# Optimization experiments

Hardware: AMD Instinct MI355X
Metric: run time of the kernel (lower is better)

## Reference

```python
import jax, jax.numpy as jnp
import numpy as np
import math

D_MODEL = 1024
EXPAND = 2
D_INNER = EXPAND * D_MODEL        # 2048
HEADDIM = 64
NHEADS = D_INNER // HEADDIM       # 32
D_STATE = 128
D_CONV = 4
CHUNK = 128
SEQLEN = 4096
BATCH = 1                         # bidirectional merge in forward hard-codes batch=1
CONV_DIM = D_INNER + 2 * (2 * D_STATE)            # 2560
D_IN_PROJ = 2 * D_INNER + 2 * (2 * D_STATE) + 2 * NHEADS  # 4672
EPS = 1e-5


def silu(x):
    return x * jax.nn.sigmoid(x)


def segsum_exp(a):
    """exp(segsum(a)): out[..., i, j] = exp(sum_{k=j+1..i} a[..., k]) for i>=j else 0."""
    T = a.shape[-1]
    m1 = jnp.tril(jnp.ones((T, T), bool), -1)
    s = jnp.cumsum(jnp.where(m1, a[..., :, None], 0.0), axis=-2)
    m0 = jnp.tril(jnp.ones((T, T), bool))
    return jnp.where(m0, jnp.exp(jnp.where(m0, s, 0.0)), 0.0)


def ssd(x, A, B, C, chunk):
    """x:(b,L,h,p) A:(b,L,h) B,C:(b,L,n) (head dim of size 1 squeezed). L % chunk == 0."""
    b, L, h, p = x.shape
    c = L // chunk
    x = x.reshape(b, c, chunk, h, p)
    A = A.reshape(b, c, chunk, h).transpose(0, 3, 1, 2)   # (b,h,c,l)
    B = B.reshape(b, c, chunk, -1)
    C = C.reshape(b, c, chunk, -1)
    A_cs = jnp.cumsum(A, axis=-1)                          # (b,h,c,l)
    Lmat = segsum_exp(A)                                   # (b,h,c,l,l)
    # intra-chunk (diagonal block) outputs
    Y_diag = jnp.einsum('bcln,bcsn,bhcls,bcshp->bclhp', C, B, Lmat, x)
    # per-chunk states
    decay_states = jnp.exp(A_cs[..., -1:] - A_cs)          # (b,h,c,l)
    states = jnp.einsum('bcln,bhcl,bclhp->bchpn', B, decay_states, x)
    states = jnp.concatenate([jnp.zeros_like(states[:, :1]), states], axis=1)
    # inter-chunk recurrence via segsum over chunk boundaries
    decay_chunk = segsum_exp(jnp.pad(A_cs[..., -1], ((0, 0), (0, 0), (1, 0))))  # (b,h,c+1,c+1)
    new_states = jnp.einsum('bhzc,bchpn->bzhpn', decay_chunk, states)
    states, final_state = new_states[:, :-1], new_states[:, -1]
    Y_off = jnp.einsum('bcln,bchpn,bhcl->bclhp', C, states, jnp.exp(A_cs))
    Y = (Y_diag + Y_off).reshape(b, L, h, p)
    return Y, final_state


def setup_inputs() -> dict:
    key = jax.random.key(0)
    ks = jax.random.split(key, 8)
    s = 0.02
    u = jax.random.normal(ks[0], (BATCH, SEQLEN, D_MODEL), jnp.float32)
    in_proj_w = jax.random.normal(ks[1], (D_IN_PROJ, D_MODEL), jnp.float32) * s
    conv_w = jax.random.normal(ks[2], (CONV_DIM, 1, D_CONV), jnp.float32) * (1.0 / math.sqrt(D_CONV))
    conv_b = jnp.zeros((CONV_DIM,), jnp.float32)
    dt = jnp.exp(jax.random.uniform(ks[3], (NHEADS,)) * (math.log(0.1) - math.log(0.001)) + math.log(0.001))
    dt = jnp.clip(dt, 1e-4)
    dt_bias = dt + jnp.log(-jnp.expm1(-dt))
    A_log = jnp.log(jax.random.uniform(ks[4], (NHEADS,), minval=1.0, maxval=16.0))
    D = jnp.ones((NHEADS,), jnp.float32)
    fc_D_w = jax.random.normal(ks[5], (NHEADS, D_INNER), jnp.float32) * s
    norm_w = jnp.ones((D_INNER,), jnp.float32)
    out_proj_w = jax.random.normal(ks[6], (D_MODEL, D_INNER), jnp.float32) * s
    return dict(u=u, in_proj_w=in_proj_w, conv_w=conv_w, conv_b=conv_b, dt_bias=dt_bias,
                A_log=A_log, D=D, fc_D_w=fc_D_w, norm_w=norm_w, out_proj_w=out_proj_w)


def reference(u, in_proj_w, conv_w, conv_b, dt_bias, A_log, D, fc_D_w, norm_w, out_proj_w):
    b, l, _ = u.shape
    zxbcdt = u @ in_proj_w.T                               # (b,l,D_IN_PROJ)
    z = zxbcdt[..., :D_INNER]
    xBC = zxbcdt[..., D_INNER:D_INNER + CONV_DIM]
    dt = zxbcdt[..., D_INNER + CONV_DIM:]                  # (b,l,2*nheads)
    # fwd heads + time-reversed bwd heads stacked on batch dim
    dt = jnp.concatenate([dt[..., :NHEADS], jnp.flip(dt[..., NHEADS:], axis=1)], axis=0)
    dt = jax.nn.softplus(dt + dt_bias)                     # (2b,l,nheads)
    # depthwise causal conv1d + silu
    xc = jnp.transpose(xBC, (0, 2, 1))                     # (b,CONV_DIM,l)
    xc = jax.lax.conv_general_dilated(xc, conv_w, (1,), [(D_CONV - 1, 0)],
                                      feature_group_count=CONV_DIM,
                                      dimension_numbers=('NCH', 'OIH', 'NCH'))
    xc = xc + conv_b[None, :, None]
    xBC = silu(jnp.transpose(xc, (0, 2, 1)))               # (b,l,CONV_DIM)
    x = xBC[..., :D_INNER]
    BC = xBC[..., D_INNER:]
    x_og = x
    x2 = jnp.concatenate([x, jnp.flip(x, 1)], axis=0)      # (2b,l,d_inner)
    BC = jnp.concatenate([BC[..., :2 * D_STATE], jnp.flip(BC[..., 2 * D_STATE:], 1)], axis=0)
    B = BC[..., :D_STATE]
    C = BC[..., D_STATE:]
    xh = x2.reshape(2 * b, l, NHEADS, HEADDIM)
    A = -jnp.exp(A_log)
    Y, final_state = ssd(xh * dt[..., None], A * dt, B, C, CHUNK)
    y = Y + xh * D[:, None]
    y = y.reshape(2 * b, l, D_INNER)
    # torch.roll(shift=1, dim=1) then zero first step == shift right with zero pad
    y = jnp.concatenate([jnp.zeros_like(y[:, :1]), y[:, :-1]], axis=1)
    y_fw, y_bw = y[:b], jnp.flip(y[b:], 1)
    fd = x_og @ fc_D_w.T + D                               # F.linear(x_og, fc_D.weight, bias=D)
    y = y_fw + y_bw + x_og * jnp.repeat(fd, HEADDIM, axis=-1)
    # gated RMSNorm
    yg = y * silu(z)
    yn = yg * jax.lax.rsqrt(jnp.mean(yg * yg, axis=-1, keepdims=True) + EPS) * norm_w
    return yn @ out_proj_w.T
```

## Files before the change

kernel.cpp:

```cpp
#include <hip/hip_runtime.h>
#include <hip/hip_bf16.h>
#include <math.h>

#define L_SEQ   4096
#define DMODEL  1024
#define DINNER  2048
#define NHEADS  32
#define HEADDIM 64
#define DSTATE  128
#define NCHUNK  32
#define CHUNKL  128
#define CONVDIM 2560
#define DPROJ   4672
#define NPAD2   4864

typedef __hip_bfloat16 bf16;
__device__ __forceinline__ float b2f(bf16 x) { return __bfloat162float(x); }
__device__ __forceinline__ bf16 f2b(float x) { return __float2bfloat16(x); }
__device__ __forceinline__ float sh2f(short s) {
  return __uint_as_float(((unsigned int)(unsigned short)s) << 16);
}
__device__ __forceinline__ short f2bs(float x) {
  bf16 t = __float2bfloat16(x);
  return *reinterpret_cast<short*>(&t);
}

typedef __attribute__((ext_vector_type(8))) short bf16x8v;
typedef __attribute__((ext_vector_type(4))) float f32x4v;

__device__ __forceinline__ float dot8(bf16x8v x, float4 w0, float4 w1) {
  return sh2f(x[0]) * w0.x + sh2f(x[1]) * w0.y + sh2f(x[2]) * w0.z + sh2f(x[3]) * w0.w +
         sh2f(x[4]) * w1.x + sh2f(x[5]) * w1.y + sh2f(x[6]) * w1.z + sh2f(x[7]) * w1.w;
}


__global__ __launch_bounds__(256) void cast2_kernel(
    const float* __restrict__ u, const float* __restrict__ w1,
    bf16* __restrict__ u_bf, bf16* __restrict__ w1_bf) {
  const int NU = (L_SEQ * DMODEL) / 256;
  int bid = blockIdx.x;
  if (bid < NU) {
    int i = bid * 256 + threadIdx.x;
    u_bf[i] = f2b(u[i]);
  } else {
    int i = (bid - NU) * 256 + threadIdx.x;
    w1_bf[i] = (i < DPROJ * DMODEL) ? f2b(w1[i]) : f2b(0.f);
  }
}

__global__ __launch_bounds__(256) void cast_kernel(
    const float* __restrict__ src, bf16* __restrict__ dst, int n_src, int n_tot) {
  int i = blockIdx.x * 256 + threadIdx.x;
  if (i < n_tot) dst[i] = (i < n_src) ? f2b(src[i]) : f2b(0.f);
}

#define G1_K  1024
#define G1_GN 19
#define G1_NT (G1_K / 64)

__global__ __launch_bounds__(512, 2) void gemm1_8ph(
    const bf16* __restrict__ A, const bf16* __restrict__ B, bf16* __restrict__ C) {
  __shared__ bf16 Al[2][2][8192];
  __shared__ bf16 Bl[2][2][8192];
  const int tid = threadIdx.x;
  const int lane = tid & 63;
  const int w = tid >> 6;
  const int wm = w >> 2;
  const int wn = w & 3;
  const int bm = (blockIdx.x / G1_GN) * 256;
  const int bn = (blockIdx.x % G1_GN) * 256;
  const int scol = ((lane & 3) ^ (((lane >> 5) & 1) << 1)) * 8;
  const int cin = ((lane >> 4) * 8) ^ (((lane >> 3) & 1) << 4);
  const int r16 = lane & 15;
  const bf16* Ag = A + (size_t)bm * G1_K;
  const bf16* Bg = B + (size_t)bn * G1_K;

  auto stage = [&](int mat, int tt, int hf) {
    const bf16* g = (mat ? Bg : Ag)
        + (size_t)(hf * 128 + (w >> 1) * 16 + (lane >> 2)) * G1_K
        + tt * 64 + (w & 1) * 32 + scol;
    bf16* d0 = mat ? &Bl[tt & 1][hf][0] : &Al[tt & 1][hf][0];
    __builtin_amdgcn_global_load_lds(
        (const __attribute__((address_space(1))) void*)g,
        (__attribute__((address_space(3))) void*)(d0 + w * 512), 16, 0, 0);
    __builtin_amdgcn_global_load_lds(
        (const __attribute__((address_space(1))) void*)(g + (size_t)64 * G1_K),
        (__attribute__((address_space(3))) void*)(d0 + (8 + w) * 512), 16, 0, 0);
  };

  f32x4v acc[8][4];
#pragma unroll
  for (int i = 0; i < 8; i++)
#pragma unroll
    for (int j = 0; j < 4; j++) acc[i][j] = (f32x4v){0.f, 0.f, 0.f, 0.f};

  stage(0, 0, 0); stage(0, 0, 1); stage(1, 0, 0); stage(1, 0, 1);
  stage(0, 1, 0); stage(0, 1, 1); stage(1, 1, 0);
  asm volatile("s_waitcnt vmcnt(6)" ::: "memory");
  __builtin_amdgcn_s_barrier();
  __builtin_amdgcn_sched_barrier(0);

#pragma unroll 2
  for (int t = 0; t < G1_NT; ++t) {
    const int slot = t & 1;
    const bf16* Ah = &Al[slot][wm][0];
    const bf16* Bh = &Bl[slot][wn >> 1][0];
    const int brb = (wn & 1) * 4;
    bf16x8v a[4][2], b[4][2];
#pragma unroll
    for (int i = 0; i < 4; i++) {
      a[i][0] = *(const bf16x8v*)&Ah[(i * 2 + 0) * 512 + r16 * 32 + cin];
      a[i][1] = *(const bf16x8v*)&Ah[(i * 2 + 1) * 512 + r16 * 32 + cin];
    }
#pragma unroll
    for (int j = 0; j < 2; j++) {
      b[j][0] = *(const bf16x8v*)&Bh[((brb + j) * 2 + 0) * 512 + r16 * 32 + cin];
      b[j][1] = *(const bf16x8v*)&Bh[((brb + j) * 2 + 1) * 512 + r16 * 32 + cin];
    }
    if (t + 1 < G1_NT) stage(1, t + 1, 1);
    __builtin_amdgcn_s_barrier();
    asm volatile("s_waitcnt lgkmcnt(0)" ::: "memory");
    __builtin_amdgcn_s_setprio(1);
#pragma unroll
    for (int i = 0; i < 4; i++)
#pragma unroll
      for (int j = 0; j < 2; j++) {
        acc[i][j] = __builtin_amdgcn_mfma_f32_16x16x32_bf16(a[i][0], b[j][0], acc[i][j], 0, 0, 0);
        acc[i][j] = __builtin_amdgcn_mfma_f32_16x16x32_bf16(a[i][1], b[j][1], acc[i][j], 0, 0, 0);
      }
    __builtin_amdgcn_s_setprio(0);
    __builtin_amdgcn_s_barrier();
#pragma unroll
    for (int j = 2; j < 4; j++) {
      b[j][0] = *(const bf16x8v*)&Bh[((brb + j) * 2 + 0) * 512 + r16 * 32 + cin];
      b[j][1] = *(const bf16x8v*)&Bh[((brb + j) * 2 + 1) * 512 + r16 * 32 + cin];
    }
    __builtin_amdgcn_s_barrier();
    asm volatile("s_waitcnt lgkmcnt(0)" ::: "memory");
    __builtin_amdgcn_s_setprio(1);
#pragma unroll
    for (int i = 0; i < 4; i++)
#pragma unroll
      for (int j = 2; j < 4; j++) {
        acc[i][j] = __builtin_amdgcn_mfma_f32_16x16x32_bf16(a[i][0], b[j][0], acc[i][j], 0, 0, 0);
        acc[i][j] = __builtin_amdgcn_mfma_f32_16x16x32_bf16(a[i][1], b[j][1], acc[i][j], 0, 0, 0);
      }
    __builtin_amdgcn_s_setprio(0);
    __builtin_amdgcn_s_barrier();
#pragma unroll
    for (int i = 0; i < 4; i++) {
      a[i][0] = *(const bf16x8v*)&Ah[((4 + i) * 2 + 0) * 512 + r16 * 32 + cin];
      a[i][1] = *(const bf16x8v*)&Ah[((4 + i) * 2 + 1) * 512 + r16 * 32 + cin];
    }
    if (t + 2 < G1_NT) stage(1, t + 2, 0);
    __builtin_amdgcn_s_barrier();
    asm volatile("s_waitcnt lgkmcnt(0)" ::: "memory");
    __builtin_amdgcn_s_setprio(1);
#pragma unroll
    for (int i = 0; i < 4; i++)
#pragma unroll
      for (int j = 2; j < 4; j++) {
        acc[4 + i][j] = __builtin_amdgcn_mfma_f32_16x16x32_bf16(a[i][0], b[j][0], acc[4 + i][j], 0, 0, 0);
        acc[4 + i][j] = __builtin_amdgcn_mfma_f32_16x16x32_bf16(a[i][1], b[j][1], acc[4 + i][j], 0, 0, 0);
      }
    __builtin_amdgcn_s_setprio(0);
    __builtin_amdgcn_s_barrier();
    if (t + 2 < G1_NT) { stage(0, t + 2, 0); stage(0, t + 2, 1); }
    __builtin_amdgcn_s_barrier();
    __builtin_amdgcn_s_setprio(1);
#pragma unroll
    for (int i = 0; i < 4; i++)
#pragma unroll
      for (int j = 0; j < 2; j++) {
        acc[4 + i][j] = __builtin_amdgcn_mfma_f32_16x16x32_bf16(a[i][0], b[j][0], acc[4 + i][j], 0, 0, 0);
        acc[4 + i][j] = __builtin_amdgcn_mfma_f32_16x16x32_bf16(a[i][1], b[j][1], acc[4 + i][j], 0, 0, 0);
      }
    __builtin_amdgcn_s_setprio(0);
    if (t < G1_NT - 2)       asm volatile("s_waitcnt vmcnt(6)" ::: "memory");
    else if (t == G1_NT - 2) asm volatile("s_waitcnt vmcnt(0)" ::: "memory");
    __builtin_amdgcn_s_barrier();
    __builtin_amdgcn_sched_barrier(0);
  }

  const int quad = lane >> 4;
  const int cn = lane & 15;
#pragma unroll
  for (int i = 0; i < 8; i++)
#pragma unroll
    for (int j = 0; j < 4; j++) {
      int col = bn + wn * 64 + j * 16 + cn;
      if (col < DPROJ) {
#pragma unroll
        for (int r = 0; r < 4; r++) {
          int row = bm + wm * 128 + i * 16 + quad * 4 + r;
          C[(size_t)row * DPROJ + col] = f2b(acc[i][j][r]);
        }
      }
    }
}

template <typename TC>
__global__ __launch_bounds__(256) void gemm_mfma(
    const bf16* __restrict__ A, int lda,
    const bf16* __restrict__ B, int ldb,
    TC* __restrict__ C, int ldc,
    int N, int K, int gridM, int gridN, int swz) {
  __shared__ short As[128][32];
  __shared__ short Bs[128][32];
  int tid = threadIdx.x;
  int lane = tid & 63;
  int w = tid >> 6;
  int wr = w >> 1, wc = w & 1;
  int bid = blockIdx.x;
  int bm, bn;
  if (swz) {
    int mst = gridM >> 3;
    int xk = bid & 7, q = bid >> 3;
    bm = (xk + 8 * (q % mst)) * 128;
    bn = (q / mst) * 128;
  } else {
    bm = (bid / gridN) * 128;
    bn = (bid % gridN) * 128;
  }
  f32x4v acc[4][4];
#pragma unroll
  for (int i = 0; i < 4; i++)
#pragma unroll
    for (int j = 0; j < 4; j++) acc[i][j] = (f32x4v){0.f, 0.f, 0.f, 0.f};

  const bf16* Ab = A + (size_t)(bm + w * 32 + (lane >> 2)) * lda + (lane & 3) * 8;
  const bf16* Bb = B + (size_t)(bn + w * 32 + (lane >> 2)) * ldb + (lane & 3) * 8;

  for (int k0 = 0; k0 < K; k0 += 32) {
    __builtin_amdgcn_global_load_lds(
        (const __attribute__((address_space(1))) void*)(Ab + k0),
        (__attribute__((address_space(3))) void*)&As[w * 32][0], 16, 0, 0);
    __builtin_amdgcn_global_load_lds(
        (const __attribute__((address_space(1))) void*)(Ab + (size_t)16 * lda + k0),
        (__attribute__((address_space(3))) void*)&As[w * 32 + 16][0], 16, 0, 0);
    __builtin_amdgcn_global_load_lds(
        (const __attribute__((address_space(1))) void*)(Bb + k0),
        (__attribute__((address_space(3))) void*)&Bs[w * 32][0], 16, 0, 0);
    __builtin_amdgcn_global_load_lds(
        (const __attribute__((address_space(1))) void*)(Bb + (size_t)16 * ldb + k0),
        (__attribute__((address_space(3))) void*)&Bs[w * 32 + 16][0], 16, 0, 0);
    __syncthreads();
    bf16x8v af[4], bv[4];
#pragma unroll
    for (int i = 0; i < 4; i++)
      af[i] = *(const bf16x8v*)&As[wr * 64 + i * 16 + (lane & 15)][(lane >> 4) * 8];
#pragma unroll
    for (int j = 0; j < 4; j++)
      bv[j] = *(const bf16x8v*)&Bs[wc * 64 + j * 16 + (lane & 15)][(lane >> 4) * 8];
#pragma unroll
    for (int i = 0; i < 4; i++)
#pragma unroll
      for (int j = 0; j < 4; j++)
        acc[i][j] = __builtin_amdgcn_mfma_f32_16x16x32_bf16(af[i], bv[j], acc[i][j], 0, 0, 0);
    __syncthreads();
  }
  int quad = lane >> 4;
  int cn = lane & 15;
#pragma unroll
  for (int i = 0; i < 4; i++) {
#pragma unroll
    for (int j = 0; j < 4; j++) {
      int col = bn + wc * 64 + j * 16 + cn;
      if (col < N) {
#pragma unroll
        for (int r = 0; r < 4; r++) {
          int row = bm + wr * 64 + i * 16 + quad * 4 + r;
          float v = acc[i][j][r];
          if constexpr (sizeof(TC) == 2) C[(size_t)row * ldc + col] = f2b(v);
          else                           C[(size_t)row * ldc + col] = v;
        }
      }
    }
  }
}

__global__ __launch_bounds__(256) void fc_kernel(
    const bf16* __restrict__ xbc, const float* __restrict__ Wf,
    const float* __restrict__ Dp, float* __restrict__ fd) {
  int lane = threadIdx.x & 63;
  int w = threadIdx.x >> 6;
  int t0 = (blockIdx.x * 4 + w) * 4;
  int h = lane & 31;
  int g = lane >> 5;
  const float* wr = Wf + (size_t)h * DINNER + g * 1024;
  const bf16* xr = xbc + (size_t)t0 * CONVDIM + g * 1024;
  float a0 = 0.f, a1 = 0.f, a2 = 0.f, a3 = 0.f;
  for (int k = 0; k < 1024; k += 8) {
    float4 w0 = *(const float4*)(wr + k);
    float4 w1 = *(const float4*)(wr + k + 4);
    bf16x8v x0 = *(const bf16x8v*)(xr + k);
    bf16x8v x1 = *(const bf16x8v*)(xr + CONVDIM + k);
    bf16x8v x2 = *(const bf16x8v*)(xr + 2 * CONVDIM + k);
    bf16x8v x3 = *(const bf16x8v*)(xr + 3 * CONVDIM + k);
    a0 += dot8(x0, w0, w1);
    a1 += dot8(x1, w0, w1);
    a2 += dot8(x2, w0, w1);
    a3 += dot8(x3, w0, w1);
  }
  a0 += __shfl_down(a0, 32);
  a1 += __shfl_down(a1, 32);
  a2 += __shfl_down(a2, 32);
  a3 += __shfl_down(a3, 32);
  if (lane < 32) {
    float d = Dp[h];
    fd[(t0 + 0) * NHEADS + h] = a0 + d;
    fd[(t0 + 1) * NHEADS + h] = a1 + d;
    fd[(t0 + 2) * NHEADS + h] = a2 + d;
    fd[(t0 + 3) * NHEADS + h] = a3 + d;
  }
}

#define CONV_BLOCKS ((L_SEQ / 4) * CONVDIM / 256)
__global__ __launch_bounds__(256) void conv_dt_kernel(
    const bf16* __restrict__ zx, const float* __restrict__ conv_w,
    const float* __restrict__ conv_b, bf16* __restrict__ xbc,
    const float* __restrict__ dt_bias, float* __restrict__ dt2) {
  int bid = blockIdx.x;
  if (bid < CONV_BLOCKS) {
    int idx = bid * 256 + threadIdx.x;
    int ch = idx % CONVDIM;
    int t0 = (idx / CONVDIM) * 4;
    const bf16* col = zx + DINNER + ch;
    float w0 = conv_w[ch * 4 + 0], w1 = conv_w[ch * 4 + 1];
    float w2 = conv_w[ch * 4 + 2], w3 = conv_w[ch * 4 + 3];
    float bsv = conv_b[ch];
    float x[7];
#pragma unroll
    for (int i = 0; i < 7; i++) {
      int t = t0 - 3 + i;
      x[i] = (t >= 0) ? b2f(col[(size_t)t * DPROJ]) : 0.f;
    }
#pragma unroll
    for (int j = 0; j < 4; j++) {
      float acc = bsv + w0 * x[j] + w1 * x[j + 1] + w2 * x[j + 2] + w3 * x[j + 3];
      xbc[(size_t)(t0 + j) * CONVDIM + ch] = f2b(acc / (1.f + __expf(-acc)));
    }
  } else {
    int idx = (bid - CONV_BLOCKS) * 256 + threadIdx.x;
    int h = idx % NHEADS;
    int t = (idx / NHEADS) % L_SEQ;
    int b = idx / (NHEADS * L_SEQ);
    float v;
    if (b == 0) v = b2f(zx[(size_t)t * DPROJ + 4608 + h]);
    else        v = b2f(zx[(size_t)(L_SEQ - 1 - t) * DPROJ + 4608 + NHEADS + h]);
    v += dt_bias[h];
    dt2[idx] = (v > 20.f) ? v : log1pf(expf(v));
  }
}

__global__ __launch_bounds__(256) void gmat_kernel(
    const bf16* __restrict__ xbc, bf16* __restrict__ G) {
  __shared__ bf16 Cs[32][136];
  __shared__ bf16 Bs[128][136];
  int blk = blockIdx.x;
  int quarter = blk & 3;
  int bc = blk >> 2;
  int b = bc / NCHUNK, c = bc % NCHUNK;
  int l0 = quarter * 32;
  int tid = threadIdx.x;
  int lane = tid & 63;
  int w = tid >> 6;
  int bofs = b ? 2304 : 2048;
  int cofs = b ? 2432 : 2176;
  for (int o = tid; o < CHUNKL * DSTATE / 8; o += 256) {
    int s = o >> 4;
    int n8 = (o & 15) * 8;
    int t = b ? (L_SEQ - 1 - (c * CHUNKL + s)) : (c * CHUNKL + s);
    *(bf16x8v*)&Bs[s][n8] = *(const bf16x8v*)&xbc[(size_t)t * CONVDIM + bofs + n8];
  }
  for (int o = tid; o < 32 * DSTATE / 8; o += 256) {
    int l = o >> 4;
    int n8 = (o & 15) * 8;
    int t = b ? (L_SEQ - 1 - (c * CHUNKL + l0 + l)) : (c * CHUNKL + l0 + l);
    *(bf16x8v*)&Cs[l][n8] = *(const bf16x8v*)&xbc[(size_t)t * CONVDIM + cofs + n8];
  }
  __syncthreads();
  if (w > quarter) return;
  f32x4v acc[2][2];
#pragma unroll
  for (int i = 0; i < 2; i++)
#pragma unroll
    for (int j = 0; j < 2; j++) acc[i][j] = (f32x4v){0.f, 0.f, 0.f, 0.f};
#pragma unroll
  for (int k0 = 0; k0 < 128; k0 += 32) {
    bf16x8v a0 = *(const bf16x8v*)&Cs[(lane & 15)][(lane >> 4) * 8 + k0];
    bf16x8v a1 = *(const bf16x8v*)&Cs[16 + (lane & 15)][(lane >> 4) * 8 + k0];
#pragma unroll
    for (int j = 0; j < 2; j++) {
      bf16x8v bv = *(const bf16x8v*)&Bs[(2 * w + j) * 16 + (lane & 15)][(lane >> 4) * 8 + k0];
      acc[0][j] = __builtin_amdgcn_mfma_f32_16x16x32_bf16(a0, bv, acc[0][j], 0, 0, 0);
      acc[1][j] = __builtin_amdgcn_mfma_f32_16x16x32_bf16(a1, bv, acc[1][j], 0, 0, 0);
    }
  }
  int quad = lane >> 4, cn = lane & 15;
  bf16* Gb = G + (size_t)bc * CHUNKL * CHUNKL;
#pragma unroll
  for (int i = 0; i < 2; i++)
#pragma unroll
    for (int j = 0; j < 2; j++)
#pragma unroll
      for (int r = 0; r < 4; r++) {
        int l = l0 + i * 16 + quad * 4 + r;
        int s = (2 * w + j) * 16 + cn;
        Gb[l * CHUNKL + s] = f2b(acc[i][j][r]);
      }
}

__global__ __launch_bounds__(256) void chunk_kernel(
    const bf16* __restrict__ xbc, const float* __restrict__ dt2,
    const float* __restrict__ A_log,
    bf16* __restrict__ states, float* __restrict__ csum) {
  int gid = blockIdx.x;
  int h = gid % NHEADS;
  int bc = gid / NHEADS;
  int c = bc % NCHUNK, b = bc / NCHUNK;
  int tid = threadIdx.x;
  int lane = tid & 63;
  int w = tid >> 6;
  __shared__ bf16 BdT[128][136];
  __shared__ bf16 xdtT[64][136];
  __shared__ float acs[CHUNKL];
  __shared__ float dtl[CHUNKL];
  __shared__ float decays[CHUNKL];
  if (tid < CHUNKL)
    dtl[tid] = dt2[((size_t)b * L_SEQ + c * CHUNKL + tid) * NHEADS + h];
  __syncthreads();
  if (tid == 0) {
    float Ah = -__expf(A_log[h]);
    float s = 0.f;
    for (int l = 0; l < CHUNKL; l++) { s += Ah * dtl[l]; acs[l] = s; }
    csum[gid] = __expf(s);
  }
  __syncthreads();
  if (tid < CHUNKL) decays[tid] = __expf(acs[CHUNKL - 1] - acs[tid]);
  for (int o = tid; o < CHUNKL * HEADDIM / 8; o += 256) {
    int s = o & 127;
    int p8 = (o >> 7) * 8;
    int t = b ? (L_SEQ - 1 - (c * CHUNKL + s)) : (c * CHUNKL + s);
    bf16x8v xv = *(const bf16x8v*)&xbc[(size_t)t * CONVDIM + h * HEADDIM + p8];
    float d = dtl[s];
#pragma unroll
    for (int j = 0; j < 8; j++) xdtT[p8 + j][s] = f2b(sh2f(xv[j]) * d);
  }
  __syncthreads();
  for (int o = tid; o < CHUNKL * CHUNKL / 8; o += 256) {
    int l = o & 127;
    int n8 = (o >> 7) * 8;
    int t = b ? (L_SEQ - 1 - (c * CHUNKL + l)) : (c * CHUNKL + l);
    bf16x8v bv = *(const bf16x8v*)&xbc[(size_t)t * CONVDIM + (b ? 2304 : 2048) + n8];
    float d = decays[l];
#pragma unroll
    for (int j = 0; j < 8; j++) BdT[n8 + j][l] = f2b(sh2f(bv[j]) * d);
  }
  __syncthreads();
  f32x4v accS[8];
#pragma unroll
  for (int j = 0; j < 8; j++) accS[j] = (f32x4v){0.f, 0.f, 0.f, 0.f};
#pragma unroll
  for (int k0 = 0; k0 < 128; k0 += 32) {
    bf16x8v av = *(const bf16x8v*)&xdtT[w * 16 + (lane & 15)][(lane >> 4) * 8 + k0];
#pragma unroll
    for (int j = 0; j < 8; j++) {
      bf16x8v bv = *(const bf16x8v*)&BdT[j * 16 + (lane & 15)][(lane >> 4) * 8 + k0];
      accS[j] = __builtin_amdgcn_mfma_f32_16x16x32_bf16(av, bv, accS[j], 0, 0, 0);
    }
  }
  int quad = lane >> 4, cn = lane & 15;
  bf16* st = states + (size_t)gid * (HEADDIM * DSTATE);
#pragma unroll
  for (int j = 0; j < 8; j++)
#pragma unroll
    for (int r = 0; r < 4; r++) {
      int p = w * 16 + quad * 4 + r;
      int n = j * 16 + cn;
      st[p * DSTATE + n] = f2b(accS[j][r]);
    }
}

__global__ __launch_bounds__(256) void scan_kernel(
    bf16* __restrict__ states, const float* __restrict__ csum) {
  int idx = blockIdx.x * 256 + threadIdx.x;
  int n = idx % DSTATE;
  int p = (idx / DSTATE) % HEADDIM;
  int h = (idx / (DSTATE * HEADDIM)) % NHEADS;
  int b = idx / (DSTATE * HEADDIM * NHEADS);
  size_t base = ((size_t)(b * NCHUNK) * NHEADS + h) * (HEADDIM * DSTATE) + p * DSTATE + n;
  const size_t cstride = (size_t)NHEADS * HEADDIM * DSTATE;
  float tmp[NCHUNK], cv[NCHUNK];
#pragma unroll
  for (int c = 0; c < NCHUNK; c++) tmp[c] = b2f(states[base + c * cstride]);
#pragma unroll
  for (int c = 0; c < NCHUNK; c++) cv[c] = csum[(b * NCHUNK + c) * NHEADS + h];
  float S = 0.f;
#pragma unroll
  for (int c = 0; c < NCHUNK; c++) {
    states[base + c * cstride] = f2b(S);
    S = cv[c] * S + tmp[c];
  }
}

__global__ __launch_bounds__(256) void yoff_kernel(
    const bf16* __restrict__ xbc, const float* __restrict__ dt2,
    const float* __restrict__ A_log, const bf16* __restrict__ G,
    const bf16* __restrict__ states, const float* __restrict__ Dp,
    bf16* __restrict__ Y) {
  int gid = blockIdx.x;
  int h = gid % NHEADS;
  int bc = gid / NHEADS;
  int c = bc % NCHUNK, b = bc / NCHUNK;
  int tid = threadIdx.x;
  int lane = tid & 63;
  int w = tid >> 6;
  __shared__ bf16 WB[128][136];
  __shared__ bf16 SX[64][136];
  __shared__ float acs[CHUNKL];
  __shared__ float dtl[CHUNKL];
  __shared__ float eAl[CHUNKL];
  if (tid < CHUNKL)
    dtl[tid] = dt2[((size_t)b * L_SEQ + c * CHUNKL + tid) * NHEADS + h];
  __syncthreads();
  if (tid == 0) {
    float Ah = -__expf(A_log[h]);
    float s = 0.f;
    for (int l = 0; l < CHUNKL; l++) { s += Ah * dtl[l]; acs[l] = s; }
  }
  __syncthreads();
  if (tid < CHUNKL) eAl[tid] = __expf(acs[tid]);
  for (int o = tid; o < CHUNKL * HEADDIM / 8; o += 256) {
    int s = o & 127;
    int p8 = (o >> 7) * 8;
    int t = b ? (L_SEQ - 1 - (c * CHUNKL + s)) : (c * CHUNKL + s);
    bf16x8v xv = *(const bf16x8v*)&xbc[(size_t)t * CONVDIM + h * HEADDIM + p8];
    float d = dtl[s];
#pragma unroll
    for (int j = 0; j < 8; j++) SX[p8 + j][s] = f2b(sh2f(xv[j]) * d);
  }
  {
    const bf16* Gb = G + (size_t)bc * CHUNKL * CHUNKL;
    for (int o = tid; o < CHUNKL * CHUNKL / 8; o += 256) {
      int l = o >> 4;
      int s8 = (o & 15) * 8;
      bf16x8v g = *(const bf16x8v*)&Gb[l * CHUNKL + s8];
      float al = acs[l];
      bf16x8v wv;
#pragma unroll
      for (int j = 0; j < 8; j++) {
        int s = s8 + j;
        float e = (s <= l) ? sh2f(g[j]) * __expf(al - acs[s]) : 0.f;
        wv[j] = f2bs(e);
      }
      *(bf16x8v*)&WB[l][s8] = wv;
    }
  }
  __syncthreads();
  f32x4v accY[2][4];
#pragma unroll
  for (int i = 0; i < 2; i++)
#pragma unroll
    for (int j = 0; j < 4; j++) accY[i][j] = (f32x4v){0.f, 0.f, 0.f, 0.f};
#pragma unroll
  for (int k0 = 0; k0 < 128; k0 += 32) {
    bf16x8v a0 = *(const bf16x8v*)&WB[w * 32 + (lane & 15)][(lane >> 4) * 8 + k0];
    bf16x8v a1 = *(const bf16x8v*)&WB[w * 32 + 16 + (lane & 15)][(lane >> 4) * 8 + k0];
#pragma unroll
    for (int j = 0; j < 4; j++) {
      bf16x8v bv = *(const bf16x8v*)&SX[j * 16 + (lane & 15)][(lane >> 4) * 8 + k0];
      accY[0][j] = __builtin_amdgcn_mfma_f32_16x16x32_bf16(a0, bv, accY[0][j], 0, 0, 0);
      accY[1][j] = __builtin_amdgcn_mfma_f32_16x16x32_bf16(a1, bv, accY[1][j], 0, 0, 0);
    }
  }
  __syncthreads();
  {
    int cofs = b ? 2432 : 2176;
    for (int o = tid; o < CHUNKL * DSTATE / 8; o += 256) {
      int l = o >> 4;
      int n8 = (o & 15) * 8;
      int t = b ? (L_SEQ - 1 - (c * CHUNKL + l)) : (c * CHUNKL + l);
      bf16x8v cv = *(const bf16x8v*)&xbc[(size_t)t * CONVDIM + cofs + n8];
      float e = eAl[l];
      bf16x8v ov;
#pragma unroll
      for (int j = 0; j < 8; j++) ov[j] = f2bs(sh2f(cv[j]) * e);
      *(bf16x8v*)&WB[l][n8] = ov;
    }
    const bf16* stp = states + (size_t)gid * (HEADDIM * DSTATE);
    for (int o = tid; o < HEADDIM * DSTATE / 8; o += 256) {
      int p = o >> 4;
      int n8 = (o & 15) * 8;
      *(bf16x8v*)&SX[p][n8] = *(const bf16x8v*)&stp[o * 8];
    }
  }
  __syncthreads();
#pragma unroll
  for (int k0 = 0; k0 < 128; k0 += 32) {
    bf16x8v a0 = *(const bf16x8v*)&WB[w * 32 + (lane & 15)][(lane >> 4) * 8 + k0];
    bf16x8v a1 = *(const bf16x8v*)&WB[w * 32 + 16 + (lane & 15)][(lane >> 4) * 8 + k0];
#pragma unroll
    for (int j = 0; j < 4; j++) {
      bf16x8v bv = *(const bf16x8v*)&SX[j * 16 + (lane & 15)][(lane >> 4) * 8 + k0];
      accY[0][j] = __builtin_amdgcn_mfma_f32_16x16x32_bf16(a0, bv, accY[0][j], 0, 0, 0);
      accY[1][j] = __builtin_amdgcn_mfma_f32_16x16x32_bf16(a1, bv, accY[1][j], 0, 0, 0);
    }
  }
  int quad = lane >> 4, cn = lane & 15;
  float Dh = Dp[h];
#pragma unroll
  for (int i = 0; i < 2; i++)
#pragma unroll
    for (int j = 0; j < 4; j++)
#pragma unroll
      for (int r = 0; r < 4; r++) {
        int l = w * 32 + i * 16 + quad * 4 + r;
        int p = j * 16 + cn;
        int t = b ? (L_SEQ - 1 - (c * CHUNKL + l)) : (c * CHUNKL + l);
        float xv = b2f(xbc[(size_t)t * CONVDIM + h * HEADDIM + p]);
        size_t yi = ((size_t)b * L_SEQ + c * CHUNKL + l) * DINNER + h * HEADDIM + p;
        Y[yi] = f2b(accY[i][j][r] + xv * Dh);
      }
}

__global__ __launch_bounds__(256) void combine_kernel(
    const bf16* __restrict__ Y, const bf16* __restrict__ xbc,
    const bf16* __restrict__ zx, const float* __restrict__ fd,
    const float* __restrict__ norm_w, bf16* __restrict__ yn) {
  int t = blockIdx.x;
  int tid = threadIdx.x;
  int j8 = tid * 8;
  float yf[8], yb[8];
#pragma unroll
  for (int j = 0; j < 8; j++) { yf[j] = 0.f; yb[j] = 0.f; }
  if (t >= 1) {
    bf16x8v v = *(const bf16x8v*)&Y[(size_t)(t - 1) * DINNER + j8];
#pragma unroll
    for (int j = 0; j < 8; j++) yf[j] = sh2f(v[j]);
  }
  if (t <= L_SEQ - 2) {
    bf16x8v v = *(const bf16x8v*)&Y[((size_t)L_SEQ + (L_SEQ - 2 - t)) * DINNER + j8];
#pragma unroll
    for (int j = 0; j < 8; j++) yb[j] = sh2f(v[j]);
  }
  bf16x8v xogv = *(const bf16x8v*)&xbc[(size_t)t * CONVDIM + j8];
  bf16x8v zv = *(const bf16x8v*)&zx[(size_t)t * DPROJ + j8];
  float fdv = fd[t * NHEADS + (j8 >> 6)];
  float yg[8];
  float ss = 0.f;
#pragma unroll
  for (int j = 0; j < 8; j++) {
    float y = yf[j] + yb[j] + sh2f(xogv[j]) * fdv;
    float z = sh2f(zv[j]);
    float g = y * (z / (1.f + __expf(-z)));
    yg[j] = g;
    ss += g * g;
  }
#pragma unroll
  for (int off = 32; off > 0; off >>= 1) ss += __shfl_down(ss, off);
  __shared__ float red[4];
  if ((tid & 63) == 0) red[tid >> 6] = ss;
  __syncthreads();
  float tot = red[0] + red[1] + red[2] + red[3];
  float scale = rsqrtf(tot / (float)DINNER + 1e-5f);
  float4 nw0 = *(const float4*)&norm_w[j8];
  float4 nw1 = *(const float4*)&norm_w[j8 + 4];
  bf16x8v ov;
  ov[0] = f2bs(yg[0] * scale * nw0.x);
  ov[1] = f2bs(yg[1] * scale * nw0.y);
  ov[2] = f2bs(yg[2] * scale * nw0.z);
  ov[3] = f2bs(yg[3] * scale * nw0.w);
  ov[4] = f2bs(yg[4] * scale * nw1.x);
  ov[5] = f2bs(yg[5] * scale * nw1.y);
  ov[6] = f2bs(yg[6] * scale * nw1.z);
  ov[7] = f2bs(yg[7] * scale * nw1.w);
  *(bf16x8v*)&yn[(size_t)t * DINNER + j8] = ov;
}

extern "C" void kernel_launch(void* const* d_in, const int* in_sizes, int n_in,
                              void* d_out, int out_size, void* d_ws, size_t ws_size,
                              hipStream_t stream) {
  const float* u         = (const float*)d_in[0];
  const float* in_proj_w = (const float*)d_in[1];
  const float* conv_w    = (const float*)d_in[2];
  const float* conv_b    = (const float*)d_in[3];
  const float* dt_bias   = (const float*)d_in[4];
  const float* A_log     = (const float*)d_in[5];
  const float* Dp        = (const float*)d_in[6];
  const float* fc_D_w    = (const float*)d_in[7];
  const float* norm_w    = (const float*)d_in[8];
  const float* out_proj_w= (const float*)d_in[9];
  float* out = (float*)d_out;

  char* base = (char*)d_ws;
  bf16*  zx  = (bf16*)base;  base += (size_t)L_SEQ * DPROJ * 2;
  bf16*  xbc = (bf16*)base;  base += (size_t)L_SEQ * CONVDIM * 2;
  float* dt2 = (float*)base; base += (size_t)2 * L_SEQ * NHEADS * 4;
  bf16*  G   = (bf16*)base;  base += (size_t)2 * NCHUNK * CHUNKL * CHUNKL * 4;
  bf16*  Yb  = (bf16*)base;  base += (size_t)2 * L_SEQ * DINNER * 4;
  bf16*  stb = (bf16*)base;  base += (size_t)2 * NCHUNK * NHEADS * HEADDIM * DSTATE * 4;
  float* cs  = (float*)base; base += (size_t)2 * NCHUNK * NHEADS * 4;
  bf16*  u_bf   = (bf16*)Yb;
  bf16*  w1p_bf = (bf16*)((char*)Yb + 9437184);
  bf16*  w2_bf  = (bf16*)G;
  bf16*  yn     = (bf16*)stb;
  float* fd     = (float*)((char*)stb + 33554432);

  cast2_kernel<<<(L_SEQ * DMODEL + NPAD2 * DMODEL) / 256, 256, 0, stream>>>(
      u, in_proj_w, u_bf, w1p_bf);
  gemm1_8ph<<<(L_SEQ / 256) * G1_GN, 512, 0, stream>>>(u_bf, w1p_bf, zx);
  conv_dt_kernel<<<CONV_BLOCKS + (2 * L_SEQ * NHEADS) / 256, 256, 0, stream>>>(
      zx, conv_w, conv_b, xbc, dt_bias, dt2);
  gmat_kernel<<<2 * NCHUNK * 4, 256, 0, stream>>>(xbc, G);
  chunk_kernel<<<2 * NCHUNK * NHEADS, 256, 0, stream>>>(
      xbc, dt2, A_log, stb, cs);
  scan_kernel<<<(2 * NHEADS * HEADDIM * DSTATE) / 256, 256, 0, stream>>>(stb, cs);
  yoff_kernel<<<2 * NCHUNK * NHEADS, 256, 0, stream>>>(
      xbc, dt2, A_log, G, stb, Dp, Yb);
  cast_kernel<<<(DMODEL * DINNER + 255) / 256, 256, 0, stream>>>(
      out_proj_w, w2_bf, DMODEL * DINNER, DMODEL * DINNER);
  fc_kernel<<<L_SEQ / 16, 256, 0, stream>>>(xbc, fc_D_w, Dp, fd);
  combine_kernel<<<L_SEQ, 256, 0, stream>>>(Yb, xbc, zx, fd, norm_w, yn);
  gemm_mfma<float><<<(L_SEQ / 128) * (DMODEL / 128), 256, 0, stream>>>(
      yn, DINNER, w2_bf, DINNER, out, DMODEL, DMODEL, DINNER,
      L_SEQ / 128, DMODEL / 128, 1);
}
```

Baseline: 415.0 us.

## Widen in_proj GEMM tile to 256x320 to reduce N padding

Changes the in_proj GEMM block tile from 256x256 to 256x320 so the padded N dimension drops from 4864 to 4800 (15 column tiles instead of 19). The LDS staging is reorganized into 64-row units, with each wave handling five 16-wide column fragments, and the load schedule and vmcnt waits are adjusted to match. This is meant to cut wasted MFMA work on padded columns and to give more reuse per A load. In exchange it raises LDS use and accumulator register pressure, which may affect occupancy at launch_bounds(512,2), and it changes the tile count relative to the CU count.

```diff
diff --git a/kernel.cpp b/kernel.cpp
--- a/kernel.cpp
+++ b/kernel.cpp
@@ -12,7 +12,7 @@
 #define CHUNKL  128
 #define CONVDIM 2560
 #define DPROJ   4672
-#define NPAD2   4864
+#define NPAD2   4800
 
 typedef __hip_bfloat16 bf16;
 __device__ __forceinline__ float b2f(bf16 x) { return __bfloat162float(x); }
@@ -55,69 +55,65 @@
 }
 
 #define G1_K  1024
-#define G1_GN 19
+#define G1_GN 15
 #define G1_NT (G1_K / 64)
 
 __global__ __launch_bounds__(512, 2) void gemm1_8ph(
     const bf16* __restrict__ A, const bf16* __restrict__ B, bf16* __restrict__ C) {
-  __shared__ bf16 Al[2][2][8192];
-  __shared__ bf16 Bl[2][2][8192];
+  __shared__ bf16 Al[2][4 * 4096];
+  __shared__ bf16 Bl[2][5 * 4096];
   const int tid = threadIdx.x;
   const int lane = tid & 63;
   const int w = tid >> 6;
   const int wm = w >> 2;
   const int wn = w & 3;
   const int bm = (blockIdx.x / G1_GN) * 256;
-  const int bn = (blockIdx.x % G1_GN) * 256;
+  const int bn = (blockIdx.x % G1_GN) * 320;
   const int scol = ((lane & 3) ^ (((lane >> 5) & 1) << 1)) * 8;
   const int cin = ((lane >> 4) * 8) ^ (((lane >> 3) & 1) << 4);
   const int r16 = lane & 15;
   const bf16* Ag = A + (size_t)bm * G1_K;
   const bf16* Bg = B + (size_t)bn * G1_K;
 
-  auto stage = [&](int mat, int tt, int hf) {
+  auto stage = [&](int mat, int tt, int u) {
     const bf16* g = (mat ? Bg : Ag)
-        + (size_t)(hf * 128 + (w >> 1) * 16 + (lane >> 2)) * G1_K
+        + (size_t)(u * 64 + (w >> 1) * 16 + (lane >> 2)) * G1_K
         + tt * 64 + (w & 1) * 32 + scol;
-    bf16* d0 = mat ? &Bl[tt & 1][hf][0] : &Al[tt & 1][hf][0];
+    bf16* d = (mat ? &Bl[tt & 1][u * 4096] : &Al[tt & 1][u * 4096]) + w * 512;
     __builtin_amdgcn_global_load_lds(
         (const __attribute__((address_space(1))) void*)g,
-        (__attribute__((address_space(3))) void*)(d0 + w * 512), 16, 0, 0);
-    __builtin_amdgcn_global_load_lds(
-        (const __attribute__((address_space(1))) void*)(g + (size_t)64 * G1_K),
-        (__attribute__((address_space(3))) void*)(d0 + (8 + w) * 512), 16, 0, 0);
+        (__attribute__((address_space(3))) void*)d, 16, 0, 0);
   };
 
-  f32x4v acc[8][4];
+  f32x4v acc[8][5];
 #pragma unroll
   for (int i = 0; i < 8; i++)
 #pragma unroll
-    for (int j = 0; j < 4; j++) acc[i][j] = (f32x4v){0.f, 0.f, 0.f, 0.f};
-
-  stage(0, 0, 0); stage(0, 0, 1); stage(1, 0, 0); stage(1, 0, 1);
-  stage(0, 1, 0); stage(0, 1, 1); stage(1, 1, 0);
-  asm volatile("s_waitcnt vmcnt(6)" ::: "memory");
+    for (int j = 0; j < 5; j++) acc[i][j] = (f32x4v){0.f, 0.f, 0.f, 0.f};
+
+  stage(0, 0, 0); stage(0, 0, 1); stage(0, 0, 2); stage(0, 0, 3);
+  stage(1, 0, 0); stage(1, 0, 1); stage(1, 0, 2); stage(1, 0, 3); stage(1, 0, 4);
+  stage(1, 1, 0); stage(1, 1, 1); stage(1, 1, 2);
+  stage(0, 1, 0); stage(0, 1, 1); stage(0, 1, 2); stage(0, 1, 3);
+  asm volatile("s_waitcnt vmcnt(7)" ::: "memory");
   __builtin_amdgcn_s_barrier();
   __builtin_amdgcn_sched_barrier(0);
 
 #pragma unroll 2
   for (int t = 0; t < G1_NT; ++t) {
     const int slot = t & 1;
-    const bf16* Ah = &Al[slot][wm][0];
-    const bf16* Bh = &Bl[slot][wn >> 1][0];
-    const int brb = (wn & 1) * 4;
-    bf16x8v a[4][2], b[4][2];
-#pragma unroll
-    for (int i = 0; i < 4; i++) {
-      a[i][0] = *(const bf16x8v*)&Ah[(i * 2 + 0) * 512 + r16 * 32 + cin];
-      a[i][1] = *(const bf16x8v*)&Ah[(i * 2 + 1) * 512 + r16 * 32 + cin];
-    }
-#pragma unroll
-    for (int j = 0; j < 2; j++) {
-      b[j][0] = *(const bf16x8v*)&Bh[((brb + j) * 2 + 0) * 512 + r16 * 32 + cin];
-      b[j][1] = *(const bf16x8v*)&Bh[((brb + j) * 2 + 1) * 512 + r16 * 32 + cin];
-    }
-    if (t + 1 < G1_NT) stage(1, t + 1, 1);
+    const bf16* As_ = &Al[slot][0];
+    const bf16* Bs_ = &Bl[slot][0];
+    bf16x8v a[4][2], b[5][2];
+#define LDA_(i, cg) (*(const bf16x8v*)&As_[(((wm * 8 + (i)) >> 2) * 4096) + \
+    ((((wm * 8 + (i)) & 3) * 2 + (cg)) * 512) + r16 * 32 + cin])
+#define LDB_(j, cg) (*(const bf16x8v*)&Bs_[(((wn * 5 + (j)) >> 2) * 4096) + \
+    ((((wn * 5 + (j)) & 3) * 2 + (cg)) * 512) + r16 * 32 + cin])
+#pragma unroll
+    for (int i = 0; i < 4; i++) { a[i][0] = LDA_(i, 0); a[i][1] = LDA_(i, 1); }
+#pragma unroll
+    for (int j = 0; j < 2; j++) { b[j][0] = LDB_(j, 0); b[j][1] = LDB_(j, 1); }
+    if (t + 1 < G1_NT) { stage(1, t + 1, 3); stage(1, t + 1, 4); }
     __builtin_amdgcn_s_barrier();
     asm volatile("s_waitcnt lgkmcnt(0)" ::: "memory");
     __builtin_amdgcn_s_setprio(1);
@@ -131,41 +127,35 @@
     __builtin_amdgcn_s_setprio(0);
     __builtin_amdgcn_s_barrier();
 #pragma unroll
-    for (int j = 2; j < 4; j++) {
-      b[j][0] = *(const bf16x8v*)&Bh[((brb + j) * 2 + 0) * 512 + r16 * 32 + cin];
-      b[j][1] = *(const bf16x8v*)&Bh[((brb + j) * 2 + 1) * 512 + r16 * 32 + cin];
-    }
+    for (int j = 2; j < 5; j++) { b[j][0] = LDB_(j, 0); b[j][1] = LDB_(j, 1); }
     __builtin_amdgcn_s_barrier();
     asm volatile("s_waitcnt lgkmcnt(0)" ::: "memory");
     __builtin_amdgcn_s_setprio(1);
 #pragma unroll
     for (int i = 0; i < 4; i++)
 #pragma unroll
-      for (int j = 2; j < 4; j++) {
+      for (int j = 2; j < 5; j++) {
         acc[i][j] = __builtin_amdgcn_mfma_f32_16x16x32_bf16(a[i][0], b[j][0], acc[i][j], 0, 0, 0);
         acc[i][j] = __builtin_amdgcn_mfma_f32_16x16x32_bf16(a[i][1], b[j][1], acc[i][j], 0, 0, 0);
       }
     __builtin_amdgcn_s_setprio(0);
     __builtin_amdgcn_s_barrier();
 #pragma unroll
-    for (int i = 0; i < 4; i++) {
-      a[i][0] = *(const bf16x8v*)&Ah[((4 + i) * 2 + 0) * 512 + r16 * 32 + cin];
-      a[i][1] = *(const bf16x8v*)&Ah[((4 + i) * 2 + 1) * 512 + r16 * 32 + cin];
-    }
-    if (t + 2 < G1_NT) stage(1, t + 2, 0);
+    for (int i = 0; i < 4; i++) { a[i][0] = LDA_(4 + i, 0); a[i][1] = LDA_(4 + i, 1); }
+    if (t + 2 < G1_NT) { stage(1, t + 2, 0); stage(1, t + 2, 1); stage(1, t + 2, 2); }
     __builtin_amdgcn_s_barrier();
     asm volatile("s_waitcnt lgkmcnt(0)" ::: "memory");
     __builtin_amdgcn_s_setprio(1);
 #pragma unroll
     for (int i = 0; i < 4; i++)
 #pragma unroll
-      for (int j = 2; j < 4; j++) {
+      for (int j = 2; j < 5; j++) {
         acc[4 + i][j] = __builtin_amdgcn_mfma_f32_16x16x32_bf16(a[i][0], b[j][0], acc[4 + i][j], 0, 0, 0);
         acc[4 + i][j] = __builtin_amdgcn_mfma_f32_16x16x32_bf16(a[i][1], b[j][1], acc[4 + i][j], 0, 0, 0);
       }
     __builtin_amdgcn_s_setprio(0);
     __builtin_amdgcn_s_barrier();
-    if (t + 2 < G1_NT) { stage(0, t + 2, 0); stage(0, t + 2, 1); }
+    if (t + 2 < G1_NT) { stage(0, t + 2, 0); stage(0, t + 2, 1); stage(0, t + 2, 2); stage(0, t + 2, 3); }
     __builtin_amdgcn_s_barrier();
     __builtin_amdgcn_s_setprio(1);
 #pragma unroll
@@ -176,10 +166,12 @@
         acc[4 + i][j] = __builtin_amdgcn_mfma_f32_16x16x32_bf16(a[i][1], b[j][1], acc[4 + i][j], 0, 0, 0);
       }
     __builtin_amdgcn_s_setprio(0);
-    if (t < G1_NT - 2)       asm volatile("s_waitcnt vmcnt(6)" ::: "memory");
+    if (t < G1_NT - 2)       asm volatile("s_waitcnt vmcnt(7)" ::: "memory");
     else if (t == G1_NT - 2) asm volatile("s_waitcnt vmcnt(0)" ::: "memory");
     __builtin_amdgcn_s_barrier();
     __builtin_amdgcn_sched_barrier(0);
+#undef LDA_
+#undef LDB_
   }
 
   const int quad = lane >> 4;
@@ -187,8 +179,8 @@
 #pragma unroll
   for (int i = 0; i < 8; i++)
 #pragma unroll
-    for (int j = 0; j < 4; j++) {
-      int col = bn + wn * 64 + j * 16 + cn;
+    for (int j = 0; j < 5; j++) {
+      int col = bn + wn * 80 + j * 16 + cn;
       if (col < DPROJ) {
 #pragma unroll
         for (int r = 0; r < 4; r++) {
```

Result: slower. 446.4 us (+7.6%).
